# Kernel optimization log

Hardware: AMD Instinct MI355X
Metric: run time of the kernel (lower is better)

## Reference

```python
import jax, jax.numpy as jnp
import numpy as np

DIM = 256
N_QUERY = 4096
N_KEY = 128
SIGMA_PRIOR = 1.0
TEMP = 1.0
LN_EPS = 1e-5


def setup_inputs() -> dict:
    key = jax.random.key(0)
    ks = jax.random.split(key, 16)
    s = 1.0 / np.sqrt(2 * DIM)
    sp = 1.0 / np.sqrt(DIM)
    return {
        "Q": jax.random.normal(ks[0], (N_QUERY, DIM), jnp.float32),
        "K": jax.random.normal(ks[1], (N_QUERY, N_KEY, DIM), jnp.float32),
        "V": jax.random.normal(ks[2], (N_QUERY, N_KEY, DIM), jnp.float32),
        "eps": jax.random.normal(ks[3], (N_QUERY, N_KEY), jnp.float32),
        # mu_posterior_layer: Linear(2*dim,1) split into Q-half and K-half
        "w_mu_q": jax.random.normal(ks[4], (DIM,), jnp.float32) * s,
        "w_mu_k": jax.random.normal(ks[5], (DIM,), jnp.float32) * s,
        "b_mu": jax.random.normal(ks[6], (), jnp.float32) * s,
        # logvar_posterior_layer: Linear(2*dim,1) split
        "w_lv_q": jax.random.normal(ks[7], (DIM,), jnp.float32) * s,
        "w_lv_k": jax.random.normal(ks[8], (DIM,), jnp.float32) * s,
        "b_lv": jax.random.normal(ks[9], (), jnp.float32) * s,
        # mu_prior_layer: Linear(dim,dim) -> ReLU -> Linear(dim,1)
        "W_pr1": jax.random.normal(ks[10], (DIM, DIM), jnp.float32) * sp,
        "b_pr1": jax.random.normal(ks[11], (DIM,), jnp.float32) * sp,
        "w_pr2": jax.random.normal(ks[12], (DIM,), jnp.float32) * sp,
        "b_pr2": jax.random.normal(ks[13], (), jnp.float32) * sp,
        # LayerNorm(dim)
        "gamma": jnp.ones((DIM,), jnp.float32),
        "beta": jnp.zeros((DIM,), jnp.float32),
    }


def reference(Q, K, V, eps, w_mu_q, w_mu_k, b_mu, w_lv_q, w_lv_k, b_lv,
              W_pr1, b_pr1, w_pr2, b_pr2, gamma, beta):
    # ---- prior: small MLP over K -> (n_query, n_key) ----
    h = jax.nn.relu(jnp.einsum('qkd,ed->qke', K, W_pr1) + b_pr1)
    mu_prior = jnp.einsum('qke,e->qk', h, w_pr2) + b_pr2
    mu_prior = mu_prior - SIGMA_PRIOR ** 2 / 2
    sigma_prior = SIGMA_PRIOR
    # ---- posterior: Linear(2*dim,1) on cat([Q_expanded, K]) == split matmuls ----
    q_mu = Q @ w_mu_q                           # (n_query,)
    q_lv = Q @ w_lv_q
    logvar_post = q_lv[:, None] + jnp.einsum('qkd,d->qk', K, w_lv_k) + b_lv
    sigma_post = jnp.exp(0.5 * logvar_post)
    mu_post = q_mu[:, None] + jnp.einsum('qkd,d->qk', K, w_mu_k) + b_mu
    mu_post = mu_post - sigma_post ** 2 / 2
    # ---- KL divergence (mean over all scores) ----
    kl = jnp.mean(jnp.log(sigma_prior / sigma_post)
                  + (sigma_post ** 2 + (mu_post - mu_prior) ** 2) / (2 * sigma_prior ** 2)
                  - 0.5)
    # ---- reparameterized sample (note: original divides by temp twice) ----
    samples = jnp.exp(mu_post + sigma_post * eps) / TEMP
    samples = samples / TEMP
    weights = jax.nn.softmax(samples, axis=-1)   # (n_query, n_key)
    # ---- weighted sum over keys + LayerNorm ----
    context = jnp.einsum('qk,qkd->qd', weights, V)
    mean = jnp.mean(context, axis=-1, keepdims=True)
    var = jnp.mean((context - mean) ** 2, axis=-1, keepdims=True)
    context = (context - mean) * jax.lax.rsqrt(var + LN_EPS) * gamma + beta
    return (context, kl)
```

## Files before the change

kernel.cpp:

```cpp
#include <hip/hip_runtime.h>
#include <hip/hip_bf16.h>
#include <stdint.h>

#define NQ 4096
#define NK 128
#define DIM 256

typedef __attribute__((ext_vector_type(4))) float f32x4;
typedef __attribute__((ext_vector_type(8))) __bf16 bf16x8;
typedef __attribute__((ext_vector_type(8))) unsigned short ushort8;

__device__ __forceinline__ unsigned short f2bf(float x) {
    union { float f; unsigned u; } v; v.f = x;
    unsigned r = v.u + 0x7FFFu + ((v.u >> 16) & 1u);
    return (unsigned short)(r >> 16);
}

__global__ void prep_pack(const float* __restrict__ Wpr1, ushort* __restrict__ Bp) {
    int t = blockIdx.x * 256 + threadIdx.x;
    int lane = t & 63;
    int fid = t >> 6;
    int h   = fid >> 6;
    int ctl = (fid >> 3) & 7;
    int kt  = fid & 7;
    int e = (h * 8 + ctl) * 16 + (lane & 15);
    int d = kt * 32 + (lane >> 4) * 8;
    const float* src = Wpr1 + (size_t)e * DIM + d;
    ushort* dst = Bp + ((size_t)fid * 64 + lane) * 8;
#pragma unroll
    for (int j = 0; j < 8; j++) dst[j] = f2bf(src[j]);
}

__global__ void prep_qdots(const float* __restrict__ Q,
                           const float* __restrict__ wmq,
                           const float* __restrict__ wlq,
                           float* __restrict__ qmu, float* __restrict__ qlv) {
    int q = blockIdx.x * 4 + (threadIdx.x >> 6);
    int lane = threadIdx.x & 63;
    const float* Qr = Q + (size_t)q * DIM;
    float dm = 0.f, dl = 0.f;
#pragma unroll
    for (int i = lane; i < DIM; i += 64) {
        float x = Qr[i];
        dm += x * wmq[i];
        dl += x * wlq[i];
    }
#pragma unroll
    for (int s = 32; s; s >>= 1) { dm += __shfl_xor(dm, s); dl += __shfl_xor(dl, s); }
    if (lane == 0) { qmu[q] = dm; qlv[q] = dl; }
}

__global__ __launch_bounds__(512, 4) void fused_main(
    const float* __restrict__ K, const float* __restrict__ V,
    const float* __restrict__ eps,
    const float* __restrict__ wmk, const float* __restrict__ bmu_p,
    const float* __restrict__ wlk, const float* __restrict__ blv_p,
    const float* __restrict__ bp1, const float* __restrict__ wp2,
    const float* __restrict__ bp2_p,
    const float* __restrict__ gamma, const float* __restrict__ beta,
    const ushort* __restrict__ Bp,
    const float* __restrict__ qmu, const float* __restrict__ qlv,
    float* __restrict__ klpart, float* __restrict__ out) {

    __shared__ __align__(16) ushort Blds[32768];
    __shared__ __align__(16) float wmk_s[DIM], wlk_s[DIM], wp2_s[DIM];
    __shared__ __align__(16) float bp1_s[DIM], gam_s[DIM], bet_s[DIM];
    __shared__ float smp_s[NK], mu_s[NK], lv_s[NK], sg_s[NK], wgt_s[NK];
    __shared__ f32x4 cpart[256];
    __shared__ float red_s[8];

    const int tid = threadIdx.x;
    const int w = tid >> 6, lane = tid & 63;
    const int q = blockIdx.x;
    const int r15 = lane & 15, g4 = lane >> 4;

    if (tid < DIM) { wmk_s[tid] = wmk[tid]; wlk_s[tid] = wlk[tid]; wp2_s[tid] = wp2[tid]; }
    else { int i = tid - DIM; bp1_s[i] = bp1[i]; gam_s[i] = gamma[i]; bet_s[i] = beta[i]; }

    {
        const uint4* src = (const uint4*)Bp;
        uint4* dst = (uint4*)Blds;
#pragma unroll
        for (int i = 0; i < 8; i++) { int f = w * 8 + i; dst[f * 64 + lane] = src[f * 64 + lane]; }
    }
    __syncthreads();

    const int row = w * 16 + r15;
    const float* Krow = K + ((size_t)q * NK + row) * DIM;
    bf16x8 afrag[8];
    float dm = 0.f, dl = 0.f;
#pragma unroll
    for (int kt = 0; kt < 8; kt++) {
        const int d0 = kt * 32 + g4 * 8;
        float4 x0 = *(const float4*)(Krow + d0);
        float4 x1 = *(const float4*)(Krow + d0 + 4);
        float4 m0 = *(const float4*)(&wmk_s[d0]);
        float4 m1 = *(const float4*)(&wmk_s[d0 + 4]);
        float4 l0 = *(const float4*)(&wlk_s[d0]);
        float4 l1 = *(const float4*)(&wlk_s[d0 + 4]);
        dm += x0.x * m0.x + x0.y * m0.y + x0.z * m0.z + x0.w * m0.w
            + x1.x * m1.x + x1.y * m1.y + x1.z * m1.z + x1.w * m1.w;
        dl += x0.x * l0.x + x0.y * l0.y + x0.z * l0.z + x0.w * l0.w
            + x1.x * l1.x + x1.y * l1.y + x1.z * l1.z + x1.w * l1.w;
        ushort8 u;
        u[0] = f2bf(x0.x); u[1] = f2bf(x0.y); u[2] = f2bf(x0.z); u[3] = f2bf(x0.w);
        u[4] = f2bf(x1.x); u[5] = f2bf(x1.y); u[6] = f2bf(x1.z); u[7] = f2bf(x1.w);
        afrag[kt] = __builtin_bit_cast(bf16x8, u);
    }
    dm += __shfl_xor(dm, 16); dm += __shfl_xor(dm, 32);
    dl += __shfl_xor(dl, 16); dl += __shfl_xor(dl, 32);

    const float b_mu = bmu_p[0], b_lv = blv_p[0], b_pr2 = bp2_p[0];
    {
        const float lv = qlv[q] + dl + b_lv;
        const float sg = expf(0.5f * lv);
        const float mp = qmu[q] + dm + b_mu - 0.5f * sg * sg;
        const float sm = expf(mp + sg * eps[(size_t)q * NK + row]);
        if (g4 == 0) { smp_s[row] = sm; mu_s[row] = mp; lv_s[row] = lv; sg_s[row] = sg; }
    }
    __syncthreads();

    if (w == 0) {
        float s0 = smp_s[lane], s1 = smp_s[64 + lane];
        float mx = fmaxf(s0, s1);
#pragma unroll
        for (int s = 32; s; s >>= 1) mx = fmaxf(mx, __shfl_xor(mx, s));
        float e0 = expf(s0 - mx), e1 = expf(s1 - mx);
        float sm = e0 + e1;
#pragma unroll
        for (int s = 32; s; s >>= 1) sm += __shfl_xor(sm, s);
        float inv = 1.f / sm;
        wgt_s[lane] = e0 * inv; wgt_s[64 + lane] = e1 * inv;
    }

    f32x4 pm = {0.f, 0.f, 0.f, 0.f};
#pragma unroll
    for (int ctl = 0; ctl < 8; ctl++) {
        f32x4 acc = {0.f, 0.f, 0.f, 0.f};
#pragma unroll
        for (int kt = 0; kt < 8; kt++) {
            ushort8 bu = *(const ushort8*)&Blds[((ctl * 8 + kt) * 64 + lane) * 8];
            acc = __builtin_amdgcn_mfma_f32_16x16x32_bf16(
                afrag[kt], __builtin_bit_cast(bf16x8, bu), acc, 0, 0, 0);
        }
        int e = ctl * 16 + r15;
        float hb = bp1_s[e], wpv = wp2_s[e];
#pragma unroll
        for (int rg = 0; rg < 4; rg++) pm[rg] += fmaxf(acc[rg] + hb, 0.f) * wpv;
    }
    __syncthreads();

    {
        const uint4* src = (const uint4*)Bp;
        uint4* dst = (uint4*)Blds;
#pragma unroll
        for (int i = 0; i < 8; i++) { int f = w * 8 + i; dst[f * 64 + lane] = src[(64 + f) * 64 + lane]; }
    }
    __syncthreads();

#pragma unroll
    for (int ctl = 0; ctl < 8; ctl++) {
        f32x4 acc = {0.f, 0.f, 0.f, 0.f};
#pragma unroll
        for (int kt = 0; kt < 8; kt++) {
            ushort8 bu = *(const ushort8*)&Blds[((ctl * 8 + kt) * 64 + lane) * 8];
            acc = __builtin_amdgcn_mfma_f32_16x16x32_bf16(
                afrag[kt], __builtin_bit_cast(bf16x8, bu), acc, 0, 0, 0);
        }
        int e = 128 + ctl * 16 + r15;
        float hb = bp1_s[e], wpv = wp2_s[e];
#pragma unroll
        for (int rg = 0; rg < 4; rg++) pm[rg] += fmaxf(acc[rg] + hb, 0.f) * wpv;
    }

#pragma unroll
    for (int s = 1; s < 16; s <<= 1) {
        pm[0] += __shfl_xor(pm[0], s); pm[1] += __shfl_xor(pm[1], s);
        pm[2] += __shfl_xor(pm[2], s); pm[3] += __shfl_xor(pm[3], s);
    }
    float klp = 0.f;
#pragma unroll
    for (int rg = 0; rg < 4; rg++) {
        int rr = w * 16 + g4 * 4 + rg;
        float mup = pm[rg] + b_pr2 - 0.5f;
        float dd = mu_s[rr] - mup;
        klp += -0.5f * lv_s[rr] + 0.5f * (sg_s[rr] * sg_s[rr] + dd * dd) - 0.5f;
    }
    klp += __shfl_xor(klp, 16); klp += __shfl_xor(klp, 32);
    if (lane == 0) red_s[w] = klp;
    __syncthreads();

    {
        f32x4 c4 = {0.f, 0.f, 0.f, 0.f};
        const f32x4* V4 = (const f32x4*)(V + (size_t)q * NK * DIM);
#pragma unroll
        for (int kk = 0; kk < 16; kk++) {
            int k = w * 16 + kk;
            float wk = wgt_s[k];
            f32x4 v = V4[k * 64 + lane];
            c4 += v * wk;
        }
        if (w >= 4) cpart[(w - 4) * 64 + lane] = c4;
        __syncthreads();
        if (w < 4) c4 += cpart[w * 64 + lane];
        __syncthreads();
        if (w == 2 || w == 3) cpart[(w - 2) * 64 + lane] = c4;
        __syncthreads();
        if (w < 2) c4 += cpart[w * 64 + lane];
        __syncthreads();
        if (w == 1) cpart[lane] = c4;
        __syncthreads();
        if (w == 0) {
            c4 += cpart[lane];
            float s1 = c4[0] + c4[1] + c4[2] + c4[3];
            float s2 = c4[0] * c4[0] + c4[1] * c4[1] + c4[2] * c4[2] + c4[3] * c4[3];
#pragma unroll
            for (int s = 32; s; s >>= 1) { s1 += __shfl_xor(s1, s); s2 += __shfl_xor(s2, s); }
            float mean = s1 * (1.f / 256.f);
            float var = s2 * (1.f / 256.f) - mean * mean;
            float rin = rsqrtf(var + 1e-5f);
            f32x4 gv = *(const f32x4*)&gam_s[lane * 4];
            f32x4 bv = *(const f32x4*)&bet_s[lane * 4];
            f32x4 o;
#pragma unroll
            for (int c = 0; c < 4; c++) o[c] = (c4[c] - mean) * rin * gv[c] + bv[c];
            *(f32x4*)(out + (size_t)q * DIM + lane * 4) = o;
        }
        if (tid == 0) {
            klpart[q] = red_s[0] + red_s[1] + red_s[2] + red_s[3]
                      + red_s[4] + red_s[5] + red_s[6] + red_s[7];
        }
    }
}

__global__ void finalize(const float* __restrict__ klpart, float* __restrict__ out) {
    __shared__ float red[4];
    int t = threadIdx.x;
    float s = 0.f;
    for (int i = t; i < NQ; i += 256) s += klpart[i];
#pragma unroll
    for (int sh = 32; sh; sh >>= 1) s += __shfl_xor(s, sh);
    if ((t & 63) == 0) red[t >> 6] = s;
    __syncthreads();
    if (t == 0) out[(size_t)NQ * DIM] = (red[0] + red[1] + red[2] + red[3]) * (1.f / ((float)NQ * NK));
}

extern "C" void kernel_launch(void* const* d_in, const int* in_sizes, int n_in,
                              void* d_out, int out_size, void* d_ws, size_t ws_size,
                              hipStream_t stream) {
    const float* Q   = (const float*)d_in[0];
    const float* K   = (const float*)d_in[1];
    const float* V   = (const float*)d_in[2];
    const float* eps = (const float*)d_in[3];
    const float* wmq = (const float*)d_in[4];
    const float* wmk = (const float*)d_in[5];
    const float* bmu = (const float*)d_in[6];
    const float* wlq = (const float*)d_in[7];
    const float* wlk = (const float*)d_in[8];
    const float* blv = (const float*)d_in[9];
    const float* Wp1 = (const float*)d_in[10];
    const float* bp1 = (const float*)d_in[11];
    const float* wp2 = (const float*)d_in[12];
    const float* bp2 = (const float*)d_in[13];
    const float* gam = (const float*)d_in[14];
    const float* bet = (const float*)d_in[15];
    float* out = (float*)d_out;

    char* ws = (char*)d_ws;
    float* qmu    = (float*)(ws + 1024);
    float* qlv    = (float*)(ws + 1024 + 16384);
    float* klpart = (float*)(ws + 1024 + 32768);
    ushort* Bp    = (ushort*)(ws + 65536);

    prep_pack<<<32, 256, 0, stream>>>(Wp1, Bp);
    prep_qdots<<<1024, 256, 0, stream>>>(Q, wmq, wlq, qmu, qlv);
    fused_main<<<NQ, 512, 0, stream>>>(K, V, eps, wmk, bmu, wlk, blv, bp1, wp2, bp2,
                                       gam, bet, Bp, qmu, qlv, klpart, out);
    finalize<<<1, 256, 0, stream>>>(klpart, out);
}
```

Measured before the change: 233.7 us.

## Alternate GEMM and V-phase order across blocks by query parity

Odd-numbered query blocks now run the V weighted-sum and LayerNorm phase before the prior-MLP MFMA GEMM, while even blocks keep the original order. Co-resident blocks on a CU should then be in different phases, so memory-bound V streaming overlaps with compute-bound MFMA work. The phase bodies are moved into macros, and a final barrier is added before the KL partial write. The odd path still depends on softmax weights computed before the branch, and both orders execute the same barriers.

Result: slower. 290.7 us (+24.4%).

```diff
diff --git a/kernel.cpp b/kernel.cpp
--- a/kernel.cpp
+++ b/kernel.cpp
@@ -49,6 +49,93 @@
     for (int s = 32; s; s >>= 1) { dm += __shfl_xor(dm, s); dl += __shfl_xor(dl, s); }
     if (lane == 0) { qmu[q] = dm; qlv[q] = dl; }
 }
+
+#define GEMM_HALF(HOFF)                                                          \
+    _Pragma("unroll")                                                            \
+    for (int ctl = 0; ctl < 8; ctl++) {                                          \
+        f32x4 acc = {0.f, 0.f, 0.f, 0.f};                                        \
+        _Pragma("unroll")                                                        \
+        for (int kt = 0; kt < 8; kt++) {                                         \
+            ushort8 bu = *(const ushort8*)&Blds[((ctl * 8 + kt) * 64 + lane) * 8];\
+            acc = __builtin_amdgcn_mfma_f32_16x16x32_bf16(                       \
+                afrag[kt], __builtin_bit_cast(bf16x8, bu), acc, 0, 0, 0);        \
+        }                                                                        \
+        int e = (HOFF) + ctl * 16 + r15;                                         \
+        float hb = bp1_s[e], wpv = wp2_s[e];                                     \
+        _Pragma("unroll")                                                        \
+        for (int rg = 0; rg < 4; rg++) pm[rg] += fmaxf(acc[rg] + hb, 0.f) * wpv; \
+    }
+
+#define RESTAGE_B_HALF1                                                          \
+    __syncthreads();                                                             \
+    {                                                                            \
+        const uint4* src = (const uint4*)Bp;                                     \
+        uint4* dst = (uint4*)Blds;                                               \
+        _Pragma("unroll")                                                        \
+        for (int i = 0; i < 8; i++) {                                            \
+            int f = w * 8 + i;                                                   \
+            dst[f * 64 + lane] = src[(64 + f) * 64 + lane];                      \
+        }                                                                        \
+    }                                                                            \
+    __syncthreads();
+
+#define KL_REDUCE                                                                \
+    _Pragma("unroll")                                                            \
+    for (int s = 1; s < 16; s <<= 1) {                                           \
+        pm[0] += __shfl_xor(pm[0], s); pm[1] += __shfl_xor(pm[1], s);            \
+        pm[2] += __shfl_xor(pm[2], s); pm[3] += __shfl_xor(pm[3], s);            \
+    }                                                                            \
+    {                                                                            \
+        float klp = 0.f;                                                         \
+        _Pragma("unroll")                                                        \
+        for (int rg = 0; rg < 4; rg++) {                                         \
+            int rr = w * 16 + g4 * 4 + rg;                                       \
+            float mup = pm[rg] + b_pr2 - 0.5f;                                   \
+            float dd = mu_s[rr] - mup;                                           \
+            klp += -0.5f * lv_s[rr] + 0.5f * (sg_s[rr] * sg_s[rr] + dd * dd) - 0.5f; \
+        }                                                                        \
+        klp += __shfl_xor(klp, 16); klp += __shfl_xor(klp, 32);                  \
+        if (lane == 0) red_s[w] = klp;                                           \
+    }
+
+#define V_PHASE                                                                  \
+    {                                                                            \
+        f32x4 c4 = {0.f, 0.f, 0.f, 0.f};                                        \
+        const f32x4* V4 = (const f32x4*)(V + (size_t)q * NK * DIM);              \
+        _Pragma("unroll")                                                        \
+        for (int kk = 0; kk < 16; kk++) {                                        \
+            int k = w * 16 + kk;                                                 \
+            float wk = wgt_s[k];                                                 \
+            f32x4 v = V4[k * 64 + lane];                                         \
+            c4 += v * wk;                                                        \
+        }                                                                        \
+        if (w >= 4) cpart[(w - 4) * 64 + lane] = c4;                             \
+        __syncthreads();                                                         \
+        if (w < 4) c4 += cpart[w * 64 + lane];                                   \
+        __syncthreads();                                                         \
+        if (w == 2 || w == 3) cpart[(w - 2) * 64 + lane] = c4;                   \
+        __syncthreads();                                                         \
+        if (w < 2) c4 += cpart[w * 64 + lane];                                   \
+        __syncthreads();                                                         \
+        if (w == 1) cpart[lane] = c4;                                            \
+        __syncthreads();                                                         \
+        if (w == 0) {                                                            \
+            c4 += cpart[lane];                                                   \
+            float s1 = c4[0] + c4[1] + c4[2] + c4[3];                            \
+            float s2 = c4[0]*c4[0] + c4[1]*c4[1] + c4[2]*c4[2] + c4[3]*c4[3];    \
+            _Pragma("unroll")                                                    \
+            for (int s = 32; s; s >>= 1) { s1 += __shfl_xor(s1, s); s2 += __shfl_xor(s2, s); } \
+            float mean = s1 * (1.f / 256.f);                                     \
+            float var = s2 * (1.f / 256.f) - mean * mean;                        \
+            float rin = rsqrtf(var + 1e-5f);                                     \
+            f32x4 gv = *(const f32x4*)&gam_s[lane * 4];                          \
+            f32x4 bv = *(const f32x4*)&bet_s[lane * 4];                          \
+            f32x4 o;                                                             \
+            _Pragma("unroll")                                                    \
+            for (int c = 0; c < 4; c++) o[c] = (c4[c] - mean) * rin * gv[c] + bv[c]; \
+            *(f32x4*)(out + (size_t)q * DIM + lane * 4) = o;                     \
+        }                                                                        \
+    }
 
 __global__ __launch_bounds__(512, 4) void fused_main(
     const float* __restrict__ K, const float* __restrict__ V,
@@ -134,102 +221,26 @@
     }
 
     f32x4 pm = {0.f, 0.f, 0.f, 0.f};
-#pragma unroll
-    for (int ctl = 0; ctl < 8; ctl++) {
-        f32x4 acc = {0.f, 0.f, 0.f, 0.f};
-#pragma unroll
-        for (int kt = 0; kt < 8; kt++) {
-            ushort8 bu = *(const ushort8*)&Blds[((ctl * 8 + kt) * 64 + lane) * 8];
-            acc = __builtin_amdgcn_mfma_f32_16x16x32_bf16(
-                afrag[kt], __builtin_bit_cast(bf16x8, bu), acc, 0, 0, 0);
-        }
-        int e = ctl * 16 + r15;
-        float hb = bp1_s[e], wpv = wp2_s[e];
-#pragma unroll
-        for (int rg = 0; rg < 4; rg++) pm[rg] += fmaxf(acc[rg] + hb, 0.f) * wpv;
-    }
-    __syncthreads();
-
-    {
-        const uint4* src = (const uint4*)Bp;
-        uint4* dst = (uint4*)Blds;
-#pragma unroll
-        for (int i = 0; i < 8; i++) { int f = w * 8 + i; dst[f * 64 + lane] = src[(64 + f) * 64 + lane]; }
-    }
-    __syncthreads();
-
-#pragma unroll
-    for (int ctl = 0; ctl < 8; ctl++) {
-        f32x4 acc = {0.f, 0.f, 0.f, 0.f};
-#pragma unroll
-        for (int kt = 0; kt < 8; kt++) {
-            ushort8 bu = *(const ushort8*)&Blds[((ctl * 8 + kt) * 64 + lane) * 8];
-            acc = __builtin_amdgcn_mfma_f32_16x16x32_bf16(
-                afrag[kt], __builtin_bit_cast(bf16x8, bu), acc, 0, 0, 0);
-        }
-        int e = 128 + ctl * 16 + r15;
-        float hb = bp1_s[e], wpv = wp2_s[e];
-#pragma unroll
-        for (int rg = 0; rg < 4; rg++) pm[rg] += fmaxf(acc[rg] + hb, 0.f) * wpv;
-    }
-
-#pragma unroll
-    for (int s = 1; s < 16; s <<= 1) {
-        pm[0] += __shfl_xor(pm[0], s); pm[1] += __shfl_xor(pm[1], s);
-        pm[2] += __shfl_xor(pm[2], s); pm[3] += __shfl_xor(pm[3], s);
-    }
-    float klp = 0.f;
-#pragma unroll
-    for (int rg = 0; rg < 4; rg++) {
-        int rr = w * 16 + g4 * 4 + rg;
-        float mup = pm[rg] + b_pr2 - 0.5f;
-        float dd = mu_s[rr] - mup;
-        klp += -0.5f * lv_s[rr] + 0.5f * (sg_s[rr] * sg_s[rr] + dd * dd) - 0.5f;
-    }
-    klp += __shfl_xor(klp, 16); klp += __shfl_xor(klp, 32);
-    if (lane == 0) red_s[w] = klp;
-    __syncthreads();
-
-    {
-        f32x4 c4 = {0.f, 0.f, 0.f, 0.f};
-        const f32x4* V4 = (const f32x4*)(V + (size_t)q * NK * DIM);
-#pragma unroll
-        for (int kk = 0; kk < 16; kk++) {
-            int k = w * 16 + kk;
-            float wk = wgt_s[k];
-            f32x4 v = V4[k * 64 + lane];
-            c4 += v * wk;
-        }
-        if (w >= 4) cpart[(w - 4) * 64 + lane] = c4;
+
+    if ((q & 1) == 0) {
+        GEMM_HALF(0)
+        RESTAGE_B_HALF1
+        GEMM_HALF(128)
+        KL_REDUCE
+        V_PHASE
+    } else {
         __syncthreads();
-        if (w < 4) c4 += cpart[w * 64 + lane];
-        __syncthreads();
-        if (w == 2 || w == 3) cpart[(w - 2) * 64 + lane] = c4;
-        __syncthreads();
-        if (w < 2) c4 += cpart[w * 64 + lane];
-        __syncthreads();
-        if (w == 1) cpart[lane] = c4;
-        __syncthreads();
-        if (w == 0) {
-            c4 += cpart[lane];
-            float s1 = c4[0] + c4[1] + c4[2] + c4[3];
-            float s2 = c4[0] * c4[0] + c4[1] * c4[1] + c4[2] * c4[2] + c4[3] * c4[3];
-#pragma unroll
-            for (int s = 32; s; s >>= 1) { s1 += __shfl_xor(s1, s); s2 += __shfl_xor(s2, s); }
-            float mean = s1 * (1.f / 256.f);
-            float var = s2 * (1.f / 256.f) - mean * mean;
-            float rin = rsqrtf(var + 1e-5f);
-            f32x4 gv = *(const f32x4*)&gam_s[lane * 4];
-            f32x4 bv = *(const f32x4*)&bet_s[lane * 4];
-            f32x4 o;
-#pragma unroll
-            for (int c = 0; c < 4; c++) o[c] = (c4[c] - mean) * rin * gv[c] + bv[c];
-            *(f32x4*)(out + (size_t)q * DIM + lane * 4) = o;
-        }
-        if (tid == 0) {
-            klpart[q] = red_s[0] + red_s[1] + red_s[2] + red_s[3]
-                      + red_s[4] + red_s[5] + red_s[6] + red_s[7];
-        }
+        V_PHASE
+        GEMM_HALF(0)
+        RESTAGE_B_HALF1
+        GEMM_HALF(128)
+        KL_REDUCE
+    }
+
+    __syncthreads();
+    if (tid == 0) {
+        klpart[q] = red_s[0] + red_s[1] + red_s[2] + red_s[3]
+                  + red_s[4] + red_s[5] + red_s[6] + red_s[7];
     }
 }
 
```

## Prefetch V rows into registers to overlap with prior-MLP MFMA work

Applied to the files above, without the earlier changes.

Issues the global loads of V for each wave's 16 keys in two batches of 8 before each half of the prior-MLP GEMM. The weighted accumulation then happens between and after the halves, so V memory latency hides behind MFMA compute instead of being a separate streaming phase at the end. Plain syncthreads are replaced with explicit lgkmcnt waits plus s_barrier and sched_barrier, which avoids waiting on the outstanding V vector-memory loads. The cost is 32 extra live VGPRs under launch_bounds(512,4), which may spill or lower occupancy.

Result: no change. 233.1 us (-0.3%).

```diff
diff --git a/kernel.cpp b/kernel.cpp
--- a/kernel.cpp
+++ b/kernel.cpp
@@ -49,6 +49,22 @@
     for (int s = 32; s; s >>= 1) { dm += __shfl_xor(dm, s); dl += __shfl_xor(dl, s); }
     if (lane == 0) { qmu[q] = dm; qlv[q] = dl; }
 }
+
+#define GEMM_HALF(HOFF)                                                          \
+    _Pragma("unroll")                                                            \
+    for (int ctl = 0; ctl < 8; ctl++) {                                          \
+        f32x4 acc = {0.f, 0.f, 0.f, 0.f};                                        \
+        _Pragma("unroll")                                                        \
+        for (int kt = 0; kt < 8; kt++) {                                         \
+            ushort8 bu = *(const ushort8*)&Blds[((ctl * 8 + kt) * 64 + lane) * 8];\
+            acc = __builtin_amdgcn_mfma_f32_16x16x32_bf16(                       \
+                afrag[kt], __builtin_bit_cast(bf16x8, bu), acc, 0, 0, 0);        \
+        }                                                                        \
+        int e = (HOFF) + ctl * 16 + r15;                                         \
+        float hb = bp1_s[e], wpv = wp2_s[e];                                     \
+        _Pragma("unroll")                                                        \
+        for (int rg = 0; rg < 4; rg++) pm[rg] += fmaxf(acc[rg] + hb, 0.f) * wpv; \
+    }
 
 __global__ __launch_bounds__(512, 4) void fused_main(
     const float* __restrict__ K, const float* __restrict__ V,
@@ -133,103 +149,110 @@
         wgt_s[lane] = e0 * inv; wgt_s[64 + lane] = e1 * inv;
     }
 
+    const f32x4* V4 = (const f32x4*)(V + (size_t)q * NK * DIM);
     f32x4 pm = {0.f, 0.f, 0.f, 0.f};
-#pragma unroll
-    for (int ctl = 0; ctl < 8; ctl++) {
-        f32x4 acc = {0.f, 0.f, 0.f, 0.f};
-#pragma unroll
-        for (int kt = 0; kt < 8; kt++) {
-            ushort8 bu = *(const ushort8*)&Blds[((ctl * 8 + kt) * 64 + lane) * 8];
-            acc = __builtin_amdgcn_mfma_f32_16x16x32_bf16(
-                afrag[kt], __builtin_bit_cast(bf16x8, bu), acc, 0, 0, 0);
-        }
-        int e = ctl * 16 + r15;
-        float hb = bp1_s[e], wpv = wp2_s[e];
-#pragma unroll
-        for (int rg = 0; rg < 4; rg++) pm[rg] += fmaxf(acc[rg] + hb, 0.f) * wpv;
-    }
-    __syncthreads();
-
+    f32x4 c4 = {0.f, 0.f, 0.f, 0.f};
+
+    f32x4 va0 = V4[(w * 16 + 0) * 64 + lane];
+    f32x4 va1 = V4[(w * 16 + 1) * 64 + lane];
+    f32x4 va2 = V4[(w * 16 + 2) * 64 + lane];
+    f32x4 va3 = V4[(w * 16 + 3) * 64 + lane];
+    f32x4 va4 = V4[(w * 16 + 4) * 64 + lane];
+    f32x4 va5 = V4[(w * 16 + 5) * 64 + lane];
+    f32x4 va6 = V4[(w * 16 + 6) * 64 + lane];
+    f32x4 va7 = V4[(w * 16 + 7) * 64 + lane];
+
+    GEMM_HALF(0)
+
+    asm volatile("s_waitcnt lgkmcnt(0)" ::: "memory");
+    __builtin_amdgcn_s_barrier();
+    __builtin_amdgcn_sched_barrier(0);
     {
         const uint4* src = (const uint4*)Bp;
         uint4* dst = (uint4*)Blds;
 #pragma unroll
         for (int i = 0; i < 8; i++) { int f = w * 8 + i; dst[f * 64 + lane] = src[(64 + f) * 64 + lane]; }
     }
-    __syncthreads();
-
-#pragma unroll
-    for (int ctl = 0; ctl < 8; ctl++) {
-        f32x4 acc = {0.f, 0.f, 0.f, 0.f};
-#pragma unroll
-        for (int kt = 0; kt < 8; kt++) {
-            ushort8 bu = *(const ushort8*)&Blds[((ctl * 8 + kt) * 64 + lane) * 8];
-            acc = __builtin_amdgcn_mfma_f32_16x16x32_bf16(
-                afrag[kt], __builtin_bit_cast(bf16x8, bu), acc, 0, 0, 0);
-        }
-        int e = 128 + ctl * 16 + r15;
-        float hb = bp1_s[e], wpv = wp2_s[e];
-#pragma unroll
-        for (int rg = 0; rg < 4; rg++) pm[rg] += fmaxf(acc[rg] + hb, 0.f) * wpv;
-    }
+    asm volatile("s_waitcnt lgkmcnt(0)" ::: "memory");
+    __builtin_amdgcn_s_barrier();
+    __builtin_amdgcn_sched_barrier(0);
+
+    c4 += va0 * wgt_s[w * 16 + 0];
+    c4 += va1 * wgt_s[w * 16 + 1];
+    c4 += va2 * wgt_s[w * 16 + 2];
+    c4 += va3 * wgt_s[w * 16 + 3];
+    c4 += va4 * wgt_s[w * 16 + 4];
+    c4 += va5 * wgt_s[w * 16 + 5];
+    c4 += va6 * wgt_s[w * 16 + 6];
+    c4 += va7 * wgt_s[w * 16 + 7];
+
+    va0 = V4[(w * 16 + 8)  * 64 + lane];
+    va1 = V4[(w * 16 + 9)  * 64 + lane];
+    va2 = V4[(w * 16 + 10) * 64 + lane];
+    va3 = V4[(w * 16 + 11) * 64 + lane];
+    va4 = V4[(w * 16 + 12) * 64 + lane];
+    va5 = V4[(w * 16 + 13) * 64 + lane];
+    va6 = V4[(w * 16 + 14) * 64 + lane];
+    va7 = V4[(w * 16 + 15) * 64 + lane];
+
+    GEMM_HALF(128)
 
 #pragma unroll
     for (int s = 1; s < 16; s <<= 1) {
         pm[0] += __shfl_xor(pm[0], s); pm[1] += __shfl_xor(pm[1], s);
         pm[2] += __shfl_xor(pm[2], s); pm[3] += __shfl_xor(pm[3], s);
     }
-    float klp = 0.f;
-#pragma unroll
-    for (int rg = 0; rg < 4; rg++) {
-        int rr = w * 16 + g4 * 4 + rg;
-        float mup = pm[rg] + b_pr2 - 0.5f;
-        float dd = mu_s[rr] - mup;
-        klp += -0.5f * lv_s[rr] + 0.5f * (sg_s[rr] * sg_s[rr] + dd * dd) - 0.5f;
-    }
-    klp += __shfl_xor(klp, 16); klp += __shfl_xor(klp, 32);
-    if (lane == 0) red_s[w] = klp;
-    __syncthreads();
-
     {
-        f32x4 c4 = {0.f, 0.f, 0.f, 0.f};
-        const f32x4* V4 = (const f32x4*)(V + (size_t)q * NK * DIM);
-#pragma unroll
-        for (int kk = 0; kk < 16; kk++) {
-            int k = w * 16 + kk;
-            float wk = wgt_s[k];
-            f32x4 v = V4[k * 64 + lane];
-            c4 += v * wk;
+        float klp = 0.f;
+#pragma unroll
+        for (int rg = 0; rg < 4; rg++) {
+            int rr = w * 16 + g4 * 4 + rg;
+            float mup = pm[rg] + b_pr2 - 0.5f;
+            float dd = mu_s[rr] - mup;
+            klp += -0.5f * lv_s[rr] + 0.5f * (sg_s[rr] * sg_s[rr] + dd * dd) - 0.5f;
         }
-        if (w >= 4) cpart[(w - 4) * 64 + lane] = c4;
-        __syncthreads();
-        if (w < 4) c4 += cpart[w * 64 + lane];
-        __syncthreads();
-        if (w == 2 || w == 3) cpart[(w - 2) * 64 + lane] = c4;
-        __syncthreads();
-        if (w < 2) c4 += cpart[w * 64 + lane];
-        __syncthreads();
-        if (w == 1) cpart[lane] = c4;
-        __syncthreads();
-        if (w == 0) {
-            c4 += cpart[lane];
-            float s1 = c4[0] + c4[1] + c4[2] + c4[3];
-            float s2 = c4[0] * c4[0] + c4[1] * c4[1] + c4[2] * c4[2] + c4[3] * c4[3];
-#pragma unroll
-            for (int s = 32; s; s >>= 1) { s1 += __shfl_xor(s1, s); s2 += __shfl_xor(s2, s); }
-            float mean = s1 * (1.f / 256.f);
-            float var = s2 * (1.f / 256.f) - mean * mean;
-            float rin = rsqrtf(var + 1e-5f);
-            f32x4 gv = *(const f32x4*)&gam_s[lane * 4];
-            f32x4 bv = *(const f32x4*)&bet_s[lane * 4];
-            f32x4 o;
-#pragma unroll
-            for (int c = 0; c < 4; c++) o[c] = (c4[c] - mean) * rin * gv[c] + bv[c];
-            *(f32x4*)(out + (size_t)q * DIM + lane * 4) = o;
-        }
-        if (tid == 0) {
-            klpart[q] = red_s[0] + red_s[1] + red_s[2] + red_s[3]
-                      + red_s[4] + red_s[5] + red_s[6] + red_s[7];
-        }
+        klp += __shfl_xor(klp, 16); klp += __shfl_xor(klp, 32);
+        if (lane == 0) red_s[w] = klp;
+    }
+
+    c4 += va0 * wgt_s[w * 16 + 8];
+    c4 += va1 * wgt_s[w * 16 + 9];
+    c4 += va2 * wgt_s[w * 16 + 10];
+    c4 += va3 * wgt_s[w * 16 + 11];
+    c4 += va4 * wgt_s[w * 16 + 12];
+    c4 += va5 * wgt_s[w * 16 + 13];
+    c4 += va6 * wgt_s[w * 16 + 14];
+    c4 += va7 * wgt_s[w * 16 + 15];
+
+    if (w >= 4) cpart[(w - 4) * 64 + lane] = c4;
+    __syncthreads();
+    if (w < 4) c4 += cpart[w * 64 + lane];
+    __syncthreads();
+    if (w == 2 || w == 3) cpart[(w - 2) * 64 + lane] = c4;
+    __syncthreads();
+    if (w < 2) c4 += cpart[w * 64 + lane];
+    __syncthreads();
+    if (w == 1) cpart[lane] = c4;
+    __syncthreads();
+    if (w == 0) {
+        c4 += cpart[lane];
+        float s1 = c4[0] + c4[1] + c4[2] + c4[3];
+        float s2 = c4[0] * c4[0] + c4[1] * c4[1] + c4[2] * c4[2] + c4[3] * c4[3];
+#pragma unroll
+        for (int s = 32; s; s >>= 1) { s1 += __shfl_xor(s1, s); s2 += __shfl_xor(s2, s); }
+        float mean = s1 * (1.f / 256.f);
+        float var = s2 * (1.f / 256.f) - mean * mean;
+        float rin = rsqrtf(var + 1e-5f);
+        f32x4 gv = *(const f32x4*)&gam_s[lane * 4];
+        f32x4 bv = *(const f32x4*)&bet_s[lane * 4];
+        f32x4 o;
+#pragma unroll
+        for (int c = 0; c < 4; c++) o[c] = (c4[c] - mean) * rin * gv[c] + bv[c];
+        *(f32x4*)(out + (size_t)q * DIM + lane * 4) = o;
+    }
+    if (tid == 0) {
+        klpart[q] = red_s[0] + red_s[1] + red_s[2] + red_s[3]
+                  + red_s[4] + red_s[5] + red_s[6] + red_s[7];
     }
 }
 
```

## Read packed prior weights directly from global memory instead of staging in LDS

Applied to the files above, without the earlier changes.

Removes the 64 KB LDS buffer that held the packed bf16 W_pr1 fragments. MFMA B-operands are now loaded straight from global memory, relying on L2/L1 caching, so the two half-staging phases and their barriers disappear. The pack layout is flattened to a single ctl index over all 256 output features, and launch bounds ask for 8 blocks per CU, which the smaller LDS footprint may allow. The tradeoff is more global/L1 traffic per MFMA and register pressure under the tighter occupancy bound.

Measured after the change: 487.1 us. +108.4%, slower.

```diff
diff --git a/kernel.cpp b/kernel.cpp
--- a/kernel.cpp
+++ b/kernel.cpp
@@ -20,10 +20,9 @@
     int t = blockIdx.x * 256 + threadIdx.x;
     int lane = t & 63;
     int fid = t >> 6;
-    int h   = fid >> 6;
-    int ctl = (fid >> 3) & 7;
+    int ctl = fid >> 3;
     int kt  = fid & 7;
-    int e = (h * 8 + ctl) * 16 + (lane & 15);
+    int e = ctl * 16 + (lane & 15);
     int d = kt * 32 + (lane >> 4) * 8;
     const float* src = Wpr1 + (size_t)e * DIM + d;
     ushort* dst = Bp + ((size_t)fid * 64 + lane) * 8;
@@ -50,7 +49,7 @@
     if (lane == 0) { qmu[q] = dm; qlv[q] = dl; }
 }
 
-__global__ __launch_bounds__(512, 4) void fused_main(
+__global__ __launch_bounds__(512, 8) void fused_main(
     const float* __restrict__ K, const float* __restrict__ V,
     const float* __restrict__ eps,
     const float* __restrict__ wmk, const float* __restrict__ bmu_p,
@@ -62,7 +61,6 @@
     const float* __restrict__ qmu, const float* __restrict__ qlv,
     float* __restrict__ klpart, float* __restrict__ out) {
 
-    __shared__ __align__(16) ushort Blds[32768];
     __shared__ __align__(16) float wmk_s[DIM], wlk_s[DIM], wp2_s[DIM];
     __shared__ __align__(16) float bp1_s[DIM], gam_s[DIM], bet_s[DIM];
     __shared__ float smp_s[NK], mu_s[NK], lv_s[NK], sg_s[NK], wgt_s[NK];
@@ -76,13 +74,6 @@
 
     if (tid < DIM) { wmk_s[tid] = wmk[tid]; wlk_s[tid] = wlk[tid]; wp2_s[tid] = wp2[tid]; }
     else { int i = tid - DIM; bp1_s[i] = bp1[i]; gam_s[i] = gamma[i]; bet_s[i] = beta[i]; }
-
-    {
-        const uint4* src = (const uint4*)Bp;
-        uint4* dst = (uint4*)Blds;
-#pragma unroll
-        for (int i = 0; i < 8; i++) { int f = w * 8 + i; dst[f * 64 + lane] = src[f * 64 + lane]; }
-    }
     __syncthreads();
 
     const int row = w * 16 + r15;
@@ -134,12 +125,13 @@
     }
 
     f32x4 pm = {0.f, 0.f, 0.f, 0.f};
-#pragma unroll
-    for (int ctl = 0; ctl < 8; ctl++) {
+    const ushort8* Bg = (const ushort8*)Bp;
+#pragma unroll
+    for (int ctl = 0; ctl < 16; ctl++) {
         f32x4 acc = {0.f, 0.f, 0.f, 0.f};
 #pragma unroll
         for (int kt = 0; kt < 8; kt++) {
-            ushort8 bu = *(const ushort8*)&Blds[((ctl * 8 + kt) * 64 + lane) * 8];
+            ushort8 bu = Bg[(ctl * 8 + kt) * 64 + lane];
             acc = __builtin_amdgcn_mfma_f32_16x16x32_bf16(
                 afrag[kt], __builtin_bit_cast(bf16x8, bu), acc, 0, 0, 0);
         }
@@ -148,88 +140,65 @@
 #pragma unroll
         for (int rg = 0; rg < 4; rg++) pm[rg] += fmaxf(acc[rg] + hb, 0.f) * wpv;
     }
-    __syncthreads();
-
-    {
-        const uint4* src = (const uint4*)Bp;
-        uint4* dst = (uint4*)Blds;
-#pragma unroll
-        for (int i = 0; i < 8; i++) { int f = w * 8 + i; dst[f * 64 + lane] = src[(64 + f) * 64 + lane]; }
-    }
-    __syncthreads();
-
-#pragma unroll
-    for (int ctl = 0; ctl < 8; ctl++) {
-        f32x4 acc = {0.f, 0.f, 0.f, 0.f};
-#pragma unroll
-        for (int kt = 0; kt < 8; kt++) {
-            ushort8 bu = *(const ushort8*)&Blds[((ctl * 8 + kt) * 64 + lane) * 8];
-            acc = __builtin_amdgcn_mfma_f32_16x16x32_bf16(
-                afrag[kt], __builtin_bit_cast(bf16x8, bu), acc, 0, 0, 0);
-        }
-        int e = 128 + ctl * 16 + r15;
-        float hb = bp1_s[e], wpv = wp2_s[e];
-#pragma unroll
-        for (int rg = 0; rg < 4; rg++) pm[rg] += fmaxf(acc[rg] + hb, 0.f) * wpv;
-    }
 
 #pragma unroll
     for (int s = 1; s < 16; s <<= 1) {
         pm[0] += __shfl_xor(pm[0], s); pm[1] += __shfl_xor(pm[1], s);
         pm[2] += __shfl_xor(pm[2], s); pm[3] += __shfl_xor(pm[3], s);
     }
-    float klp = 0.f;
-#pragma unroll
-    for (int rg = 0; rg < 4; rg++) {
-        int rr = w * 16 + g4 * 4 + rg;
-        float mup = pm[rg] + b_pr2 - 0.5f;
-        float dd = mu_s[rr] - mup;
-        klp += -0.5f * lv_s[rr] + 0.5f * (sg_s[rr] * sg_s[rr] + dd * dd) - 0.5f;
-    }
-    klp += __shfl_xor(klp, 16); klp += __shfl_xor(klp, 32);
-    if (lane == 0) red_s[w] = klp;
-    __syncthreads();
-
     {
-        f32x4 c4 = {0.f, 0.f, 0.f, 0.f};
-        const f32x4* V4 = (const f32x4*)(V + (size_t)q * NK * DIM);
-#pragma unroll
-        for (int kk = 0; kk < 16; kk++) {
-            int k = w * 16 + kk;
-            float wk = wgt_s[k];
-            f32x4 v = V4[k * 64 + lane];
-            c4 += v * wk;
+        float klp = 0.f;
+#pragma unroll
+        for (int rg = 0; rg < 4; rg++) {
+            int rr = w * 16 + g4 * 4 + rg;
+            float mup = pm[rg] + b_pr2 - 0.5f;
+            float dd = mu_s[rr] - mup;
+            klp += -0.5f * lv_s[rr] + 0.5f * (sg_s[rr] * sg_s[rr] + dd * dd) - 0.5f;
         }
-        if (w >= 4) cpart[(w - 4) * 64 + lane] = c4;
-        __syncthreads();
-        if (w < 4) c4 += cpart[w * 64 + lane];
-        __syncthreads();
-        if (w == 2 || w == 3) cpart[(w - 2) * 64 + lane] = c4;
-        __syncthreads();
-        if (w < 2) c4 += cpart[w * 64 + lane];
-        __syncthreads();
-        if (w == 1) cpart[lane] = c4;
-        __syncthreads();
-        if (w == 0) {
-            c4 += cpart[lane];
-            float s1 = c4[0] + c4[1] + c4[2] + c4[3];
-            float s2 = c4[0] * c4[0] + c4[1] * c4[1] + c4[2] * c4[2] + c4[3] * c4[3];
-#pragma unroll
-            for (int s = 32; s; s >>= 1) { s1 += __shfl_xor(s1, s); s2 += __shfl_xor(s2, s); }
-            float mean = s1 * (1.f / 256.f);
-            float var = s2 * (1.f / 256.f) - mean * mean;
-            float rin = rsqrtf(var + 1e-5f);
-            f32x4 gv = *(const f32x4*)&gam_s[lane * 4];
-            f32x4 bv = *(const f32x4*)&bet_s[lane * 4];
-            f32x4 o;
-#pragma unroll
-            for (int c = 0; c < 4; c++) o[c] = (c4[c] - mean) * rin * gv[c] + bv[c];
-            *(f32x4*)(out + (size_t)q * DIM + lane * 4) = o;
-        }
-        if (tid == 0) {
-            klpart[q] = red_s[0] + red_s[1] + red_s[2] + red_s[3]
-                      + red_s[4] + red_s[5] + red_s[6] + red_s[7];
-        }
+        klp += __shfl_xor(klp, 16); klp += __shfl_xor(klp, 32);
+        if (lane == 0) red_s[w] = klp;
+    }
+    __syncthreads();
+
+    f32x4 c4 = {0.f, 0.f, 0.f, 0.f};
+    const f32x4* V4 = (const f32x4*)(V + (size_t)q * NK * DIM);
+#pragma unroll
+    for (int kk = 0; kk < 16; kk++) {
+        int k = w * 16 + kk;
+        float wk = wgt_s[k];
+        f32x4 v = V4[k * 64 + lane];
+        c4 += v * wk;
+    }
+
+    if (w >= 4) cpart[(w - 4) * 64 + lane] = c4;
+    __syncthreads();
+    if (w < 4) c4 += cpart[w * 64 + lane];
+    __syncthreads();
+    if (w == 2 || w == 3) cpart[(w - 2) * 64 + lane] = c4;
+    __syncthreads();
+    if (w < 2) c4 += cpart[w * 64 + lane];
+    __syncthreads();
+    if (w == 1) cpart[lane] = c4;
+    __syncthreads();
+    if (w == 0) {
+        c4 += cpart[lane];
+        float s1 = c4[0] + c4[1] + c4[2] + c4[3];
+        float s2 = c4[0] * c4[0] + c4[1] * c4[1] + c4[2] * c4[2] + c4[3] * c4[3];
+#pragma unroll
+        for (int s = 32; s; s >>= 1) { s1 += __shfl_xor(s1, s); s2 += __shfl_xor(s2, s); }
+        float mean = s1 * (1.f / 256.f);
+        float var = s2 * (1.f / 256.f) - mean * mean;
+        float rin = rsqrtf(var + 1e-5f);
+        f32x4 gv = *(const f32x4*)&gam_s[lane * 4];
+        f32x4 bv = *(const f32x4*)&bet_s[lane * 4];
+        f32x4 o;
+#pragma unroll
+        for (int c = 0; c < 4; c++) o[c] = (c4[c] - mean) * rin * gv[c] + bv[c];
+        *(f32x4*)(out + (size_t)q * DIM + lane * 4) = o;
+    }
+    if (tid == 0) {
+        klpart[q] = red_s[0] + red_s[1] + red_s[2] + red_s[3]
+                  + red_s[4] + red_s[5] + red_s[6] + red_s[7];
     }
 }
 
```
